# Optimization experiments

Hardware: AMD Instinct MI355X
Metric: run time of the kernel (lower is better)

## Reference

```python
import jax, jax.numpy as jnp
import numpy as np

N, E, R, H, FDIM, OUT = 50000, 800000, 12, 128, 1582, 2
Q = H // 4  # 32
SLOPE = 0.01  # LeakyReLU default negative slope


def leaky(x):
    return jnp.where(x > 0, x, SLOPE * x)


def rgcn(x, src, dst, etype, W, root, bias):
    # Per-relation mean aggregation of neighbor features, then linear transform
    # (PyG RGCNConv default aggr='mean'). Linear => transform-then-mean is equal.
    # count of edges of each (relation, dst) pair
    seg = etype * N + dst
    cnt = jnp.zeros((R * N,), x.dtype).at[seg].add(1.0)
    norm = 1.0 / jnp.maximum(cnt[seg], 1.0)          # [E]
    xw = jnp.einsum('nh,rhd->nrd', x, W)             # [N,R,H] per-relation transform
    msg = xw[src, etype] * norm[:, None]             # [E,H] gather + normalize
    agg = jax.ops.segment_sum(msg, dst, num_segments=N)  # [N,H] scatter-add
    return agg + x @ root + bias


def setup_inputs() -> dict:
    key = jax.random.key(0)
    ks = jax.random.split(key, 16)
    s = lambda d: 1.0 / np.sqrt(d)
    inp = {
        'feature': jax.random.normal(ks[0], (N, FDIM), jnp.float32),
        'edge_index': jax.random.randint(ks[1], (2, E), 0, N),
        'edge_type': jax.random.randint(ks[2], (E,), 0, R),
        'W_des': jax.random.normal(ks[3], (768, Q), jnp.float32) * s(768),
        'b_des': jnp.zeros((Q,), jnp.float32),
        'W_tweet': jax.random.normal(ks[4], (768, Q), jnp.float32) * s(768),
        'b_tweet': jnp.zeros((Q,), jnp.float32),
        'W_num': jax.random.normal(ks[5], (34, Q), jnp.float32) * s(34),
        'b_num': jnp.zeros((Q,), jnp.float32),
        'W_cat': jax.random.normal(ks[6], (12, Q), jnp.float32) * s(12),
        'b_cat': jnp.zeros((Q,), jnp.float32),
        'W_in': jax.random.normal(ks[7], (H, H), jnp.float32) * s(H),
        'b_in': jnp.zeros((H,), jnp.float32),
        'rgcn_W': jax.random.normal(ks[8], (R, H, H), jnp.float32) * s(H),
        'rgcn_root': jax.random.normal(ks[9], (H, H), jnp.float32) * s(H),
        'rgcn_bias': jnp.zeros((H,), jnp.float32),
        'W_out1': jax.random.normal(ks[10], (H, H), jnp.float32) * s(H),
        'b_out1': jnp.zeros((H,), jnp.float32),
        'W_out2': jax.random.normal(ks[11], (H, OUT), jnp.float32) * s(H),
        'b_out2': jnp.zeros((OUT,), jnp.float32),
    }
    return inp


def reference(feature, edge_index, edge_type, W_des, b_des, W_tweet, b_tweet,
              W_num, b_num, W_cat, b_cat, W_in, b_in, rgcn_W, rgcn_root,
              rgcn_bias, W_out1, b_out1, W_out2, b_out2):
    src, dst = edge_index[0], edge_index[1]
    d = leaky(feature[:, -1536:-768] @ W_des + b_des)
    t = leaky(feature[:, -768:] @ W_tweet + b_tweet)
    num = leaky(feature[:, 12:46] @ W_num + b_num)
    cat = leaky(feature[:, 0:12] @ W_cat + b_cat)
    x = jnp.concatenate((d, t, num, cat), axis=1)       # [N,H]
    x = leaky(x @ W_in + b_in)
    x = rgcn(x, src, dst, edge_type, rgcn_W, rgcn_root, rgcn_bias)
    # dropout: identity in eval mode (deterministic reference)
    x = rgcn(x, src, dst, edge_type, rgcn_W, rgcn_root, rgcn_bias)
    x = leaky(x @ W_out1 + b_out1)
    return x @ W_out2 + b_out2
```

## Files before the change

kernel.cpp:

```cpp
#include <hip/hip_runtime.h>
#include <stdint.h>

#define NN 50000
#define NE 800000
#define NR 12
#define NH 128
#define NF 1582
#define NSEG (NN * NR)
#define MT 3125
#define SCAN_NB ((NSEG + 255) / 256)
#define KSENC 50
#define KSSTK 52

typedef __attribute__((ext_vector_type(8))) short short8;
typedef __attribute__((ext_vector_type(4))) float floatx4;

__device__ __forceinline__ float bf2f(unsigned int u16) {
    union { unsigned int i; float f; } w; w.i = u16 << 16; return w.f;
}
__device__ __forceinline__ unsigned short f2bf(float f) {
    union { float f; unsigned int i; } w; w.f = f;
    unsigned int i = w.i;
    return (unsigned short)((i + 0x7FFFu + ((i >> 16) & 1u)) >> 16);
}
__device__ __forceinline__ float leaky_f(float v) { return v > 0.f ? v : 0.01f * v; }

__global__ __launch_bounds__(256) void swz_k(
    const float* __restrict__ src1, int K1,
    const float* __restrict__ src2, int Ktot, int N, int KS,
    unsigned short* __restrict__ dst)
{
    const int idx = blockIdx.x * 256 + threadIdx.x;
    const int total = (N >> 4) * KS * 512;
    if (idx >= total) return;
    const int j = idx & 7;
    const int lane = (idx >> 3) & 63;
    const int cks = idx >> 9;
    const int ks = cks % KS;
    const int ct = cks / KS;
    const int k = ks * 32 + (lane >> 4) * 8 + j;
    const int col = ct * 16 + (lane & 15);
    float v = 0.f;
    if (k < Ktot) v = (k < K1) ? src1[(size_t)k * N + col] : src2[(size_t)(k - K1) * N + col];
    dst[idx] = f2bf(v);
}

__global__ __launch_bounds__(256) void swzenc_k(
    const float* __restrict__ Wdes, const float* __restrict__ Wtw,
    const float* __restrict__ Wnum, const float* __restrict__ Wcat,
    unsigned short* __restrict__ dst)
{
    const int idx = blockIdx.x * 256 + threadIdx.x;
    const int total = 8 * KSENC * 512;
    if (idx >= total) return;
    const int j = idx & 7;
    const int lane = (idx >> 3) & 63;
    const int cks = idx >> 9;
    const int ks = cks % KSENC;
    const int ct = cks / KSENC;
    const int k = ks * 32 + (lane >> 4) * 8 + j;
    const int col = ct * 16 + (lane & 15);
    float v = 0.f;
    if (col < 32) {
        if (k >= 46 && k < 814)   v = Wdes[(size_t)(k - 46) * 32 + col];
    } else if (col < 64) {
        if (k >= 814 && k < 1582) v = Wtw[(size_t)(k - 814) * 32 + (col - 32)];
    } else if (col < 96) {
        if (k >= 12 && k < 46)    v = Wnum[(size_t)(k - 12) * 32 + (col - 64)];
    } else {
        if (k < 12)               v = Wcat[(size_t)k * 32 + (col - 96)];
    }
    dst[idx] = f2bf(v);
}

__global__ __launch_bounds__(128) void packbias_k(
    const float* __restrict__ bdes, const float* __restrict__ btw,
    const float* __restrict__ bnum, const float* __restrict__ bcat,
    float* __restrict__ be)
{
    const int c = threadIdx.x;
    float v;
    if (c < 32) v = bdes[c];
    else if (c < 64) v = btw[c - 32];
    else if (c < 96) v = bnum[c - 64];
    else v = bcat[c - 96];
    be[c] = v;
}

__global__ __launch_bounds__(256) void hist_k(const int* __restrict__ dst,
                                              const int* __restrict__ et,
                                              int* __restrict__ deg)
{
    const int e = blockIdx.x * 256 + threadIdx.x;
    if (e >= NE) return;
    atomicAdd(&deg[dst[e] * NR + et[e]], 1);
}

__global__ __launch_bounds__(256) void scanA_k(const int* __restrict__ deg,
                                               int* __restrict__ offs,
                                               int* __restrict__ part)
{
    __shared__ int lds[256];
    const int i = blockIdx.x * 256 + threadIdx.x;
    const int v = (i < NSEG) ? deg[i] : 0;
    lds[threadIdx.x] = v; __syncthreads();
#pragma unroll
    for (int d = 1; d < 256; d <<= 1) {
        const int t = (threadIdx.x >= d) ? lds[threadIdx.x - d] : 0;
        __syncthreads();
        lds[threadIdx.x] += t;
        __syncthreads();
    }
    if (i < NSEG) offs[i] = lds[threadIdx.x] - v;
    if (threadIdx.x == 255) part[blockIdx.x] = lds[255];
}

__global__ __launch_bounds__(256) void scanB_k(int* __restrict__ part, int nb)
{
    __shared__ int lds[256];
    __shared__ int carry;
    if (threadIdx.x == 0) carry = 0;
    __syncthreads();
    for (int base = 0; base < nb; base += 256) {
        const int i = base + threadIdx.x;
        const int v = (i < nb) ? part[i] : 0;
        lds[threadIdx.x] = v; __syncthreads();
#pragma unroll
        for (int d = 1; d < 256; d <<= 1) {
            const int t = (threadIdx.x >= d) ? lds[threadIdx.x - d] : 0;
            __syncthreads();
            lds[threadIdx.x] += t;
            __syncthreads();
        }
        if (i < nb) part[i] = lds[threadIdx.x] - v + carry;
        __syncthreads();
        if (threadIdx.x == 255) carry += lds[255];
        __syncthreads();
    }
}

__global__ __launch_bounds__(256) void scanC_k(int* __restrict__ offs,
                                               const int* __restrict__ part)
{
    const int i = blockIdx.x * 256 + threadIdx.x;
    if (i < NSEG) offs[i] += part[blockIdx.x];
}

__global__ __launch_bounds__(256) void fill_k(const int* __restrict__ src,
                                              const int* __restrict__ dst,
                                              const int* __restrict__ et,
                                              const int* __restrict__ offs,
                                              int* __restrict__ cur,
                                              unsigned int* __restrict__ eidx)
{
    const int e = blockIdx.x * 256 + threadIdx.x;
    if (e >= NE) return;
    const int s = dst[e] * NR + et[e];
    const int pos = offs[s] + atomicAdd(&cur[s], 1);
    eidx[pos] = (unsigned int)src[e];
}

__global__ __launch_bounds__(256) void enc_k(
    const float* __restrict__ feat,
    const unsigned short* __restrict__ Benc, const float* __restrict__ be,
    const unsigned short* __restrict__ Bwin, const float* __restrict__ bin,
    unsigned short* __restrict__ xa)
{
    const int wave = threadIdx.x >> 6, lane = threadIdx.x & 63;
    const int q = lane >> 4, cl = lane & 15;
    int tile = blockIdx.x * 4 + wave;
    if (tile >= MT) tile = MT - 1;
    const int row = tile * 16 + cl;

    const int lo[8] = {1, 1, 25, 25, 0, 0, 0, 0};
    const int hi[8] = {26, 26, 50, 50, 2, 2, 1, 1};

    floatx4 acc[8];
#pragma unroll
    for (int ct = 0; ct < 8; ct++) { floatx4 z = {0.f,0.f,0.f,0.f}; acc[ct] = z; }

    for (int ks = 0; ks < KSENC; ks++) {
        const int kb = ks * 32 + q * 8;
        union { short8 v; unsigned short u[8]; } a;
        const float* ap = feat + (size_t)row * NF + kb;
        if (kb + 7 < NF) {
#pragma unroll
            for (int j = 0; j < 4; j++) {
                const float2 t = *(const float2*)__builtin_assume_aligned(ap + 2 * j, 8);
                a.u[2 * j]     = f2bf(t.x);
                a.u[2 * j + 1] = f2bf(t.y);
            }
        } else {
#pragma unroll
            for (int j = 0; j < 8; j++)
                a.u[j] = ((kb + j) < NF) ? f2bf(ap[j]) : 0;
        }
#pragma unroll
        for (int ct = 0; ct < 8; ct++) {
            if (ks >= lo[ct] && ks < hi[ct]) {
                const short8 b = *(const short8*)(Benc + ((size_t)(ct * KSENC + ks) * 64 + lane) * 8);
                acc[ct] = __builtin_amdgcn_mfma_f32_16x16x32_bf16(a.v, b, acc[ct], 0, 0, 0);
            }
        }
    }

    __shared__ unsigned short lds[4][16][136];
#pragma unroll
    for (int ct = 0; ct < 8; ct++) {
        const int col = ct * 16 + cl;
        const float bv = be[col];
#pragma unroll
        for (int r = 0; r < 4; r++)
            lds[wave][q * 4 + r][col] = f2bf(leaky_f(acc[ct][r] + bv));
    }
    __syncthreads();

    floatx4 acc2[8];
#pragma unroll
    for (int ct = 0; ct < 8; ct++) { floatx4 z = {0.f,0.f,0.f,0.f}; acc2[ct] = z; }
#pragma unroll
    for (int ks2 = 0; ks2 < 4; ks2++) {
        const short8 a2 = *(const short8*)&lds[wave][cl][ks2 * 32 + q * 8];
#pragma unroll
        for (int ct = 0; ct < 8; ct++) {
            const short8 b = *(const short8*)(Bwin + ((size_t)(ct * 4 + ks2) * 64 + lane) * 8);
            acc2[ct] = __builtin_amdgcn_mfma_f32_16x16x32_bf16(a2, b, acc2[ct], 0, 0, 0);
        }
    }
#pragma unroll
    for (int ct = 0; ct < 8; ct++) {
        const int col = ct * 16 + cl;
        const float bv = bin[col];
#pragma unroll
        for (int r = 0; r < 4; r++)
            xa[(size_t)(tile * 16 + q * 4 + r) * NH + col] = f2bf(leaky_f(acc2[ct][r] + bv));
    }
}

__global__ __launch_bounds__(256) void layer_k(
    const unsigned short* __restrict__ xin,
    const unsigned int* __restrict__ eidx,
    const int* __restrict__ offs, const int* __restrict__ deg,
    const unsigned short* __restrict__ Bstk, const float* __restrict__ rbias,
    unsigned short* __restrict__ xout)
{
    const int wave = threadIdx.x >> 6, lane = threadIdx.x & 63;
    const int q = lane >> 4, cl = lane & 15;
    const int tile = blockIdx.x * 4 + wave;
    if (tile >= MT) return;
    const int d = tile * 16 + cl;

    floatx4 acc[8];
#pragma unroll
    for (int ct = 0; ct < 8; ct++) { floatx4 z = {0.f,0.f,0.f,0.f}; acc[ct] = z; }

    for (int r = 0; r < NR; r++) {
        const int seg = d * NR + r;
        const int beg = offs[seg];
        const int n = deg[seg];
        float f[4][8];
#pragma unroll
        for (int ki = 0; ki < 4; ki++)
#pragma unroll
            for (int m = 0; m < 8; m++) f[ki][m] = 0.f;

        for (int e = 0; e < n; e++) {
            const unsigned int nb = eidx[beg + e];
            const unsigned short* xr = xin + (size_t)nb * NH + q * 8;
#pragma unroll
            for (int ki = 0; ki < 4; ki++) {
                const uint4 t = *(const uint4*)(xr + ki * 32);
                f[ki][0] += bf2f(t.x & 0xFFFFu); f[ki][1] += bf2f(t.x >> 16);
                f[ki][2] += bf2f(t.y & 0xFFFFu); f[ki][3] += bf2f(t.y >> 16);
                f[ki][4] += bf2f(t.z & 0xFFFFu); f[ki][5] += bf2f(t.z >> 16);
                f[ki][6] += bf2f(t.w & 0xFFFFu); f[ki][7] += bf2f(t.w >> 16);
            }
        }
        const float w = 1.0f / (float)(n > 1 ? n : 1);
#pragma unroll
        for (int ki = 0; ki < 4; ki++) {
            union { short8 v; unsigned short u[8]; } a;
#pragma unroll
            for (int m = 0; m < 8; m++) a.u[m] = f2bf(f[ki][m] * w);
            const int ks = r * 4 + ki;
#pragma unroll
            for (int ct = 0; ct < 8; ct++) {
                const short8 b = *(const short8*)(Bstk + ((size_t)(ct * KSSTK + ks) * 64 + lane) * 8);
                acc[ct] = __builtin_amdgcn_mfma_f32_16x16x32_bf16(a.v, b, acc[ct], 0, 0, 0);
            }
        }
    }

#pragma unroll
    for (int ki = 0; ki < 4; ki++) {
        const short8 a = *(const short8*)__builtin_assume_aligned(
            xin + (size_t)d * NH + ki * 32 + q * 8, 16);
        const int ks = 48 + ki;
#pragma unroll
        for (int ct = 0; ct < 8; ct++) {
            const short8 b = *(const short8*)(Bstk + ((size_t)(ct * KSSTK + ks) * 64 + lane) * 8);
            acc[ct] = __builtin_amdgcn_mfma_f32_16x16x32_bf16(a, b, acc[ct], 0, 0, 0);
        }
    }

#pragma unroll
    for (int ct = 0; ct < 8; ct++) {
        const int col = ct * 16 + cl;
        const float bv = rbias[col];
#pragma unroll
        for (int r2 = 0; r2 < 4; r2++)
            xout[(size_t)(tile * 16 + q * 4 + r2) * NH + col] = f2bf(acc[ct][r2] + bv);
    }
}

__global__ __launch_bounds__(256) void head_k(
    const unsigned short* __restrict__ xa,
    const unsigned short* __restrict__ Bo1, const float* __restrict__ bo1,
    const float* __restrict__ Wo2, const float* __restrict__ bo2,
    float* __restrict__ out)
{
    const int wave = threadIdx.x >> 6, lane = threadIdx.x & 63;
    const int q = lane >> 4, cl = lane & 15;
    int tile = blockIdx.x * 4 + wave;
    if (tile >= MT) tile = MT - 1;

    floatx4 acc[8];
#pragma unroll
    for (int ct = 0; ct < 8; ct++) { floatx4 z = {0.f,0.f,0.f,0.f}; acc[ct] = z; }
#pragma unroll
    for (int ks = 0; ks < 4; ks++) {
        const short8 a = *(const short8*)__builtin_assume_aligned(
            xa + (size_t)(tile * 16 + cl) * NH + ks * 32 + q * 8, 16);
#pragma unroll
        for (int ct = 0; ct < 8; ct++) {
            const short8 b = *(const short8*)(Bo1 + ((size_t)(ct * 4 + ks) * 64 + lane) * 8);
            acc[ct] = __builtin_amdgcn_mfma_f32_16x16x32_bf16(a, b, acc[ct], 0, 0, 0);
        }
    }
    __shared__ unsigned short lds[4][16][136];
#pragma unroll
    for (int ct = 0; ct < 8; ct++) {
        const int col = ct * 16 + cl;
        const float bv = bo1[col];
#pragma unroll
        for (int r = 0; r < 4; r++)
            lds[wave][q * 4 + r][col] = f2bf(leaky_f(acc[ct][r] + bv));
    }
    __syncthreads();

    if (lane < 32) {
        const int row = lane >> 1, o = lane & 1;
        float s = bo2[o];
        for (int k = 0; k < NH; k++)
            s += bf2f(lds[wave][row][k]) * Wo2[k * 2 + o];
        out[(size_t)(tile * 16 + row) * 2 + o] = s;
    }
}

extern "C" void kernel_launch(void* const* d_in, const int* in_sizes, int n_in,
                              void* d_out, int out_size, void* d_ws, size_t ws_size,
                              hipStream_t stream)
{
    const float* feat = (const float*)d_in[0];
    const int* ei   = (const int*)d_in[1];
    const int* et   = (const int*)d_in[2];
    const float* Wdes = (const float*)d_in[3];
    const float* bdes = (const float*)d_in[4];
    const float* Wtw  = (const float*)d_in[5];
    const float* btw  = (const float*)d_in[6];
    const float* Wnum = (const float*)d_in[7];
    const float* bnum = (const float*)d_in[8];
    const float* Wcat = (const float*)d_in[9];
    const float* bcat = (const float*)d_in[10];
    const float* Win  = (const float*)d_in[11];
    const float* bin  = (const float*)d_in[12];
    const float* rgW  = (const float*)d_in[13];
    const float* root = (const float*)d_in[14];
    const float* rbias= (const float*)d_in[15];
    const float* Wo1  = (const float*)d_in[16];
    const float* bo1  = (const float*)d_in[17];
    const float* Wo2  = (const float*)d_in[18];
    const float* bo2  = (const float*)d_in[19];
    const int* srcp = ei;
    const int* dstp = ei + NE;

    char* p = (char*)d_ws;
    auto alloc = [&](size_t bytes) { char* r = p; p += (bytes + 255) & ~(size_t)255; return r; };
    unsigned short* xa = (unsigned short*)alloc((size_t)NN * NH * 2);
    unsigned short* xb = (unsigned short*)alloc((size_t)NN * NH * 2);
    int* deg  = (int*)alloc((size_t)NSEG * 4);
    int* offs = (int*)alloc((size_t)NSEG * 4);
    int* cur  = (int*)alloc((size_t)NSEG * 4);
    int* part = (int*)alloc((size_t)(SCAN_NB + 8) * 4);
    unsigned int* eidx = (unsigned int*)alloc((size_t)NE * 4);
    unsigned short* Benc = (unsigned short*)alloc((size_t)8 * KSENC * 512 * 2);
    unsigned short* sWin = (unsigned short*)alloc((size_t)8 * 4 * 512 * 2);
    unsigned short* sWstk= (unsigned short*)alloc((size_t)8 * KSSTK * 512 * 2);
    unsigned short* sWo1 = (unsigned short*)alloc((size_t)8 * 4 * 512 * 2);
    float* be = (float*)alloc(128 * 4);

    const int GB = (MT + 3) / 4;

    hipMemsetAsync(deg, 0, (size_t)NSEG * 4, stream);
    hipMemsetAsync(cur, 0, (size_t)NSEG * 4, stream);
    hist_k<<<(NE + 255) / 256, 256, 0, stream>>>(dstp, et, deg);
    scanA_k<<<SCAN_NB, 256, 0, stream>>>(deg, offs, part);
    scanB_k<<<1, 256, 0, stream>>>(part, SCAN_NB);
    scanC_k<<<SCAN_NB, 256, 0, stream>>>(offs, part);
    fill_k<<<(NE + 255) / 256, 256, 0, stream>>>(srcp, dstp, et, offs, cur, eidx);

    swzenc_k<<<(8 * KSENC * 512 + 255) / 256, 256, 0, stream>>>(Wdes, Wtw, Wnum, Wcat, Benc);
    packbias_k<<<1, 128, 0, stream>>>(bdes, btw, bnum, bcat, be);
    swz_k<<<(8 * 4 * 512 + 255) / 256, 256, 0, stream>>>(Win, 128, Win, 128, 128, 4, sWin);
    swz_k<<<(8 * KSSTK * 512 + 255) / 256, 256, 0, stream>>>(rgW, 1536, root, 1664, 128, KSSTK, sWstk);
    swz_k<<<(8 * 4 * 512 + 255) / 256, 256, 0, stream>>>(Wo1, 128, Wo1, 128, 128, 4, sWo1);

    enc_k<<<GB, 256, 0, stream>>>(feat, Benc, be, sWin, bin, xa);
    layer_k<<<GB, 256, 0, stream>>>(xa, eidx, offs, deg, sWstk, rbias, xb);
    layer_k<<<GB, 256, 0, stream>>>(xb, eidx, offs, deg, sWstk, rbias, xa);
    head_k<<<GB, 256, 0, stream>>>(xa, sWo1, bo1, Wo2, bo2, (float*)d_out);
}
```

Measured before the change: 938.1 us.

## Transform-then-gather RGCN: precompute per-relation XW, gather weighted rows per node

Each RGCN layer is split into an MFMA kernel that computes X·W_r for all 12 relations plus root into a [N,13,128] bf16 buffer, and a gather kernel that sums the pre-transformed rows over all incoming edges of a node, weighting each by the reciprocal degree. The edge index packs src*13+relation together with a clamped segment degree, so each node needs one contiguous edge loop instead of twelve per-relation loops followed by MFMAs. The change removes the per-relation aggregation-then-matmul structure and its irregular inner loops. In exchange it writes and reads a 13x wider intermediate (about 166MB) and rounds messages to bf16 before summing; the 20-bit index and 12-bit degree packing limit the sizes it can handle.

```diff
diff --git a/kernel.cpp b/kernel.cpp
--- a/kernel.cpp
+++ b/kernel.cpp
@@ -4,13 +4,15 @@
 #define NN 50000
 #define NE 800000
 #define NR 12
+#define NRX 13
 #define NH 128
 #define NF 1582
 #define NSEG (NN * NR)
 #define MT 3125
+#define MT2 1563
 #define SCAN_NB ((NSEG + 255) / 256)
 #define KSENC 50
-#define KSSTK 52
+#define CTXW (NRX * 8)
 
 typedef __attribute__((ext_vector_type(8))) short short8;
 typedef __attribute__((ext_vector_type(4))) float floatx4;
@@ -24,6 +26,9 @@
     return (unsigned short)((i + 0x7FFFu + ((i >> 16) & 1u)) >> 16);
 }
 __device__ __forceinline__ float leaky_f(float v) { return v > 0.f ? v : 0.01f * v; }
+__device__ __forceinline__ float fast_rcp(float x) {
+    float r; asm("v_rcp_f32 %0, %1" : "=v"(r) : "v"(x)); return r;
+}
 
 __global__ __launch_bounds__(256) void swz_k(
     const float* __restrict__ src1, int K1,
@@ -42,6 +47,27 @@
     const int col = ct * 16 + (lane & 15);
     float v = 0.f;
     if (k < Ktot) v = (k < K1) ? src1[(size_t)k * N + col] : src2[(size_t)(k - K1) * N + col];
+    dst[idx] = f2bf(v);
+}
+
+__global__ __launch_bounds__(256) void swzxw_k(
+    const float* __restrict__ rgW, const float* __restrict__ root,
+    unsigned short* __restrict__ dst)
+{
+    const int idx = blockIdx.x * 256 + threadIdx.x;
+    const int total = CTXW * 4 * 512;
+    if (idx >= total) return;
+    const int j = idx & 7;
+    const int lane = (idx >> 3) & 63;
+    const int cks = idx >> 9;
+    const int ks = cks & 3;
+    const int ctg = cks >> 2;
+    const int r = ctg >> 3;
+    const int ct8 = ctg & 7;
+    const int k = ks * 32 + (lane >> 4) * 8 + j;
+    const int c = ct8 * 16 + (lane & 15);
+    const float v = (r < NR) ? rgW[((size_t)r * NH + k) * NH + c]
+                             : root[(size_t)k * NH + c];
     dst[idx] = f2bf(v);
 }
 
@@ -150,14 +176,17 @@
                                               const int* __restrict__ dst,
                                               const int* __restrict__ et,
                                               const int* __restrict__ offs,
+                                              const int* __restrict__ deg,
                                               int* __restrict__ cur,
                                               unsigned int* __restrict__ eidx)
 {
     const int e = blockIdx.x * 256 + threadIdx.x;
     if (e >= NE) return;
-    const int s = dst[e] * NR + et[e];
+    const int r = et[e];
+    const int s = dst[e] * NR + r;
     const int pos = offs[s] + atomicAdd(&cur[s], 1);
-    eidx[pos] = (unsigned int)src[e];
+    int n = deg[s]; if (n > 4095) n = 4095;
+    eidx[pos] = (unsigned int)(src[e] * NRX + r) | ((unsigned int)n << 20);
 }
 
 __global__ __launch_bounds__(256) void enc_k(
@@ -237,11 +266,60 @@
     }
 }
 
-__global__ __launch_bounds__(256) void layer_k(
+__global__ __launch_bounds__(256) void xw_k(
     const unsigned short* __restrict__ xin,
+    const unsigned short* __restrict__ Bxw,
+    unsigned short* __restrict__ xw)
+{
+    const int wave = threadIdx.x >> 6, lane = threadIdx.x & 63;
+    const int q = lane >> 4, cl = lane & 15;
+    const int wid = blockIdx.x * 4 + wave;
+    if (wid >= MT2 * NRX) return;
+    const int t2 = wid / NRX;
+    const int r = wid - t2 * NRX;
+    const int ta = t2 * 2;
+    const int tb = (ta + 1 < MT) ? ta + 1 : MT - 1;
+
+    floatx4 accA[8], accB[8];
+#pragma unroll
+    for (int ct = 0; ct < 8; ct++) {
+        floatx4 z = {0.f,0.f,0.f,0.f}; accA[ct] = z; accB[ct] = z;
+    }
+#pragma unroll
+    for (int ks = 0; ks < 4; ks++) {
+        const short8 aA = *(const short8*)__builtin_assume_aligned(
+            xin + (size_t)(ta * 16 + cl) * NH + ks * 32 + q * 8, 16);
+        const short8 aB = *(const short8*)__builtin_assume_aligned(
+            xin + (size_t)(tb * 16 + cl) * NH + ks * 32 + q * 8, 16);
+#pragma unroll
+        for (int ct = 0; ct < 8; ct++) {
+            const short8 b = *(const short8*)(Bxw + ((size_t)((r * 8 + ct) * 4 + ks) * 64 + lane) * 8);
+            accA[ct] = __builtin_amdgcn_mfma_f32_16x16x32_bf16(aA, b, accA[ct], 0, 0, 0);
+            accB[ct] = __builtin_amdgcn_mfma_f32_16x16x32_bf16(aB, b, accB[ct], 0, 0, 0);
+        }
+    }
+#pragma unroll
+    for (int ct = 0; ct < 8; ct++) {
+        const int col = ct * 16 + cl;
+#pragma unroll
+        for (int rr = 0; rr < 4; rr++) {
+            xw[((size_t)(ta * 16 + q * 4 + rr) * NRX + r) * NH + col] = f2bf(accA[ct][rr]);
+            xw[((size_t)(tb * 16 + q * 4 + rr) * NRX + r) * NH + col] = f2bf(accB[ct][rr]);
+        }
+    }
+}
+
+#define ACC8(fk, t, w) \
+    fk[0] += (w) * bf2f(t.x & 0xFFFFu); fk[1] += (w) * bf2f(t.x >> 16); \
+    fk[2] += (w) * bf2f(t.y & 0xFFFFu); fk[3] += (w) * bf2f(t.y >> 16); \
+    fk[4] += (w) * bf2f(t.z & 0xFFFFu); fk[5] += (w) * bf2f(t.z >> 16); \
+    fk[6] += (w) * bf2f(t.w & 0xFFFFu); fk[7] += (w) * bf2f(t.w >> 16);
+
+__global__ __launch_bounds__(256) void gather_k(
+    const unsigned short* __restrict__ xw,
     const unsigned int* __restrict__ eidx,
-    const int* __restrict__ offs, const int* __restrict__ deg,
-    const unsigned short* __restrict__ Bstk, const float* __restrict__ rbias,
+    const int* __restrict__ offs,
+    const float* __restrict__ rbias,
     unsigned short* __restrict__ xout)
 {
     const int wave = threadIdx.x >> 6, lane = threadIdx.x & 63;
@@ -249,67 +327,42 @@
     const int tile = blockIdx.x * 4 + wave;
     if (tile >= MT) return;
     const int d = tile * 16 + cl;
-
-    floatx4 acc[8];
-#pragma unroll
-    for (int ct = 0; ct < 8; ct++) { floatx4 z = {0.f,0.f,0.f,0.f}; acc[ct] = z; }
-
-    for (int r = 0; r < NR; r++) {
-        const int seg = d * NR + r;
-        const int beg = offs[seg];
-        const int n = deg[seg];
-        float f[4][8];
-#pragma unroll
-        for (int ki = 0; ki < 4; ki++)
-#pragma unroll
-            for (int m = 0; m < 8; m++) f[ki][m] = 0.f;
-
-        for (int e = 0; e < n; e++) {
-            const unsigned int nb = eidx[beg + e];
-            const unsigned short* xr = xin + (size_t)nb * NH + q * 8;
-#pragma unroll
-            for (int ki = 0; ki < 4; ki++) {
-                const uint4 t = *(const uint4*)(xr + ki * 32);
-                f[ki][0] += bf2f(t.x & 0xFFFFu); f[ki][1] += bf2f(t.x >> 16);
-                f[ki][2] += bf2f(t.y & 0xFFFFu); f[ki][3] += bf2f(t.y >> 16);
-                f[ki][4] += bf2f(t.z & 0xFFFFu); f[ki][5] += bf2f(t.z >> 16);
-                f[ki][6] += bf2f(t.w & 0xFFFFu); f[ki][7] += bf2f(t.w >> 16);
-            }
-        }
-        const float w = 1.0f / (float)(n > 1 ? n : 1);
+    const int beg = offs[d * NR];
+    const int end = (d < NN - 1) ? offs[(d + 1) * NR] : NE;
+
+    float f[4][8];
+    {
+        const unsigned short* xr = xw + ((size_t)d * NRX + NR) * NH + q * 8;
 #pragma unroll
         for (int ki = 0; ki < 4; ki++) {
-            union { short8 v; unsigned short u[8]; } a;
-#pragma unroll
-            for (int m = 0; m < 8; m++) a.u[m] = f2bf(f[ki][m] * w);
-            const int ks = r * 4 + ki;
-#pragma unroll
-            for (int ct = 0; ct < 8; ct++) {
-                const short8 b = *(const short8*)(Bstk + ((size_t)(ct * KSSTK + ks) * 64 + lane) * 8);
-                acc[ct] = __builtin_amdgcn_mfma_f32_16x16x32_bf16(a.v, b, acc[ct], 0, 0, 0);
-            }
-        }
+            const uint4 t = *(const uint4*)(xr + ki * 32);
+            f[ki][0] = bf2f(t.x & 0xFFFFu); f[ki][1] = bf2f(t.x >> 16);
+            f[ki][2] = bf2f(t.y & 0xFFFFu); f[ki][3] = bf2f(t.y >> 16);
+            f[ki][4] = bf2f(t.z & 0xFFFFu); f[ki][5] = bf2f(t.z >> 16);
+            f[ki][6] = bf2f(t.w & 0xFFFFu); f[ki][7] = bf2f(t.w >> 16);
+        }
+    }
+
+    unsigned int vnext = (beg < end) ? eidx[beg] : 0u;
+    for (int e = beg; e < end; ++e) {
+        const unsigned int val = vnext;
+        if (e + 1 < end) vnext = eidx[e + 1];
+        const float w = fast_rcp((float)(val >> 20));
+        const unsigned short* xr = xw + (size_t)(val & 0xFFFFFu) * NH + q * 8;
+        const uint4 t0 = *(const uint4*)(xr);
+        const uint4 t1 = *(const uint4*)(xr + 32);
+        const uint4 t2 = *(const uint4*)(xr + 64);
+        const uint4 t3 = *(const uint4*)(xr + 96);
+        ACC8(f[0], t0, w); ACC8(f[1], t1, w); ACC8(f[2], t2, w); ACC8(f[3], t3, w);
     }
 
 #pragma unroll
     for (int ki = 0; ki < 4; ki++) {
-        const short8 a = *(const short8*)__builtin_assume_aligned(
-            xin + (size_t)d * NH + ki * 32 + q * 8, 16);
-        const int ks = 48 + ki;
-#pragma unroll
-        for (int ct = 0; ct < 8; ct++) {
-            const short8 b = *(const short8*)(Bstk + ((size_t)(ct * KSSTK + ks) * 64 + lane) * 8);
-            acc[ct] = __builtin_amdgcn_mfma_f32_16x16x32_bf16(a, b, acc[ct], 0, 0, 0);
-        }
-    }
-
-#pragma unroll
-    for (int ct = 0; ct < 8; ct++) {
-        const int col = ct * 16 + cl;
-        const float bv = rbias[col];
-#pragma unroll
-        for (int r2 = 0; r2 < 4; r2++)
-            xout[(size_t)(tile * 16 + q * 4 + r2) * NH + col] = f2bf(acc[ct][r2] + bv);
+        union { short8 v; unsigned short u[8]; } o;
+#pragma unroll
+        for (int m = 0; m < 8; m++)
+            o.u[m] = f2bf(f[ki][m] + rbias[ki * 32 + q * 8 + m]);
+        *(short8*)(xout + (size_t)d * NH + ki * 32 + q * 8) = o.v;
     }
 }
 
@@ -395,11 +448,13 @@
     unsigned int* eidx = (unsigned int*)alloc((size_t)NE * 4);
     unsigned short* Benc = (unsigned short*)alloc((size_t)8 * KSENC * 512 * 2);
     unsigned short* sWin = (unsigned short*)alloc((size_t)8 * 4 * 512 * 2);
-    unsigned short* sWstk= (unsigned short*)alloc((size_t)8 * KSSTK * 512 * 2);
+    unsigned short* Bxw  = (unsigned short*)alloc((size_t)CTXW * 4 * 512 * 2);
     unsigned short* sWo1 = (unsigned short*)alloc((size_t)8 * 4 * 512 * 2);
     float* be = (float*)alloc(128 * 4);
+    unsigned short* xwbuf = (unsigned short*)alloc((size_t)NN * NRX * NH * 2);
 
     const int GB = (MT + 3) / 4;
+    const int GBXW = (MT2 * NRX + 3) / 4;
 
     hipMemsetAsync(deg, 0, (size_t)NSEG * 4, stream);
     hipMemsetAsync(cur, 0, (size_t)NSEG * 4, stream);
@@ -407,16 +462,18 @@
     scanA_k<<<SCAN_NB, 256, 0, stream>>>(deg, offs, part);
     scanB_k<<<1, 256, 0, stream>>>(part, SCAN_NB);
     scanC_k<<<SCAN_NB, 256, 0, stream>>>(offs, part);
-    fill_k<<<(NE + 255) / 256, 256, 0, stream>>>(srcp, dstp, et, offs, cur, eidx);
+    fill_k<<<(NE + 255) / 256, 256, 0, stream>>>(srcp, dstp, et, offs, deg, cur, eidx);
 
     swzenc_k<<<(8 * KSENC * 512 + 255) / 256, 256, 0, stream>>>(Wdes, Wtw, Wnum, Wcat, Benc);
     packbias_k<<<1, 128, 0, stream>>>(bdes, btw, bnum, bcat, be);
     swz_k<<<(8 * 4 * 512 + 255) / 256, 256, 0, stream>>>(Win, 128, Win, 128, 128, 4, sWin);
-    swz_k<<<(8 * KSSTK * 512 + 255) / 256, 256, 0, stream>>>(rgW, 1536, root, 1664, 128, KSSTK, sWstk);
+    swzxw_k<<<(CTXW * 4 * 512 + 255) / 256, 256, 0, stream>>>(rgW, root, Bxw);
     swz_k<<<(8 * 4 * 512 + 255) / 256, 256, 0, stream>>>(Wo1, 128, Wo1, 128, 128, 4, sWo1);
 
     enc_k<<<GB, 256, 0, stream>>>(feat, Benc, be, sWin, bin, xa);
-    layer_k<<<GB, 256, 0, stream>>>(xa, eidx, offs, deg, sWstk, rbias, xb);
-    layer_k<<<GB, 256, 0, stream>>>(xb, eidx, offs, deg, sWstk, rbias, xa);
+    xw_k<<<GBXW, 256, 0, stream>>>(xa, Bxw, xwbuf);
+    gather_k<<<GB, 256, 0, stream>>>(xwbuf, eidx, offs, rbias, xb);
+    xw_k<<<GBXW, 256, 0, stream>>>(xb, Bxw, xwbuf);
+    gather_k<<<GB, 256, 0, stream>>>(xwbuf, eidx, offs, rbias, xa);
     head_k<<<GB, 256, 0, stream>>>(xa, sWo1, bo1, Wo2, bo2, (float*)d_out);
 }
```

New measurement: 863.4 us. 1.09x faster.
